# Kernel tuning notes

Hardware: AMD Instinct MI355X
Metric: run time of the kernel (lower is better)

## Reference

```python
import jax, jax.numpy as jnp
import numpy as np

NH, HS = 12, 64            # num heads, head size
H = NH * HS                # hidden size 768
SCALE = 1.0 / np.sqrt(HS)


def binary_quant(x):
    # BinaryQuantizer forward: sign(x)
    return jnp.sign(x)


def zmean_binary_quant(x):
    # ZMeanBinaryQuantizer forward: (sign(x)+1)/2 in {0,1}
    return (jnp.sign(x) + 1.0) * 0.5


def quant_weight(w):
    # 1-bit weight: per-output-row scale * sign(w)
    s = jnp.mean(jnp.abs(w), axis=1, keepdims=True)
    return s * jnp.sign(w)


def setup_inputs() -> dict:
    key = jax.random.key(0)
    ks = jax.random.split(key, 8)
    B, S = 16, 512
    return {
        "hidden_states": jax.random.normal(ks[0], (B, S, H), dtype=jnp.float32),
        "attention_mask": jnp.zeros((B, 1, 1, S), dtype=jnp.float32),
        "Wq": jax.random.normal(ks[1], (H, H), dtype=jnp.float32) * 0.02,
        "bq": jax.random.normal(ks[2], (H,), dtype=jnp.float32) * 0.02,
        "Wk": jax.random.normal(ks[3], (H, H), dtype=jnp.float32) * 0.02,
        "bk": jax.random.normal(ks[4], (H,), dtype=jnp.float32) * 0.02,
        "Wv": jax.random.normal(ks[5], (H, H), dtype=jnp.float32) * 0.02,
        "bv": jax.random.normal(ks[6], (H,), dtype=jnp.float32) * 0.02,
    }


def reference(hidden_states, attention_mask, Wq, bq, Wk, bk, Wv, bv):
    B, S, _ = hidden_states.shape

    def lin(x, W, b):  # F.linear with 1-bit weight
        return x @ quant_weight(W).T + b

    def heads(x):  # [B,S,H] -> [B,NH,S,HS]
        return x.reshape(B, S, NH, HS).transpose(0, 2, 1, 3)

    q = heads(lin(hidden_states, Wq, bq))
    k = heads(lin(hidden_states, Wk, bk))
    v = heads(lin(hidden_states, Wv, bv))

    query_scores = jnp.einsum('bhqd,bhkd->bhqk', q, q) * SCALE
    key_scores = jnp.einsum('bhqd,bhkd->bhqk', k, k) * SCALE

    qb = binary_quant(q)
    kb = binary_quant(k)
    attention_scores = jnp.einsum('bhqd,bhkd->bhqk', qb, kb) * SCALE + attention_mask

    value_scores = jnp.einsum('bhqd,bhkd->bhqk', v, v) * SCALE

    # dropout in eval mode = identity
    attention_probs = zmean_binary_quant(attention_scores)
    vb = binary_quant(v)

    context = jnp.einsum('bhqk,bhkd->bhqd', attention_probs, vb)
    context = context.transpose(0, 2, 1, 3).reshape(B, S, H)
    return (context, attention_scores, value_scores, query_scores, key_scores)
```

## Files before the change

kernel.cpp:

```cpp
#include <hip/hip_runtime.h>
#include <cstdint>

#define B__ 16
#define S__ 512
#define NH__ 12
#define HS__ 64
#define H__ 768
#define BH__ 192
#define M__ 8192
#define K__ 768
#define N3__ 2304
#define PLANE__ 6291456
#define QKV_ELEMS__ 6291456

typedef int    int4v   __attribute__((ext_vector_type(4)));
typedef short  short8  __attribute__((ext_vector_type(8)));
typedef float  float4v __attribute__((ext_vector_type(4)));

__device__ __forceinline__ unsigned short f2bf(float f) {
    unsigned u = __float_as_uint(f);
    u += 0x7fffu + ((u >> 16) & 1u);
    return (unsigned short)(u >> 16);
}

__global__ __launch_bounds__(256)
void prep_w_kernel(const float* __restrict__ Wq, const float* __restrict__ Wk,
                   const float* __restrict__ Wv,
                   double* __restrict__ scales, signed char* __restrict__ sgnW) {
    int wid = threadIdx.x >> 6, lane = threadIdx.x & 63;
    int row = blockIdx.x * 4 + wid;
    if (row >= N3__) return;
    int w = row / 768, i = row - w * 768;
    const float* W = (w == 0) ? Wq : ((w == 1) ? Wk : Wv);
    const float* wr = W + (size_t)i * 768;
    double s = 0.0;
    #pragma unroll
    for (int j = 0; j < 12; j++) {
        float x = wr[lane + j * 64];
        s += fabs((double)x);
        sgnW[(size_t)row * 768 + lane + j * 64] =
            (signed char)((x > 0.f) - (x < 0.f));
    }
    #pragma unroll
    for (int off = 32; off; off >>= 1) s += __shfl_down(s, off);
    if (lane == 0) scales[row] = s * (1.0 / 768.0);
}

__global__ __launch_bounds__(256)
void prep_x_kernel(const float* __restrict__ hs, signed char* __restrict__ planes) {
    int idx = blockIdx.x * 256 + threadIdx.x;
    float x = hs[idx];
    double d = (double)x * 268435456.0;
    d = fmin(fmax(d, -2130706400.0), 2130706400.0);
    int v = __double2int_rn(d);
    int d0 = (int)(signed char)(v & 0xff);
    int r1 = (v - d0) >> 8;
    int d1 = (int)(signed char)(r1 & 0xff);
    int r2 = (r1 - d1) >> 8;
    int d2 = (int)(signed char)(r2 & 0xff);
    int r3 = (r2 - d2) >> 8;
    planes[idx]               = (signed char)d0;
    planes[PLANE__ + idx]     = (signed char)d1;
    planes[2 * PLANE__ + idx] = (signed char)d2;
    planes[3 * PLANE__ + idx] = (signed char)r3;
}

__global__ __launch_bounds__(256)
void proj_kernel(const signed char* __restrict__ planes,
                 const signed char* __restrict__ sgnW,
                 const double* __restrict__ scales,
                 const float* __restrict__ bq, const float* __restrict__ bk,
                 const float* __restrict__ bv,
                 unsigned short* __restrict__ qkv,
                 signed char* __restrict__ qb, signed char* __restrict__ kb,
                 signed char* __restrict__ vbT) {
    int wid = threadIdx.x >> 6, lane = threadIdx.x & 63;
    int lrow = lane & 15, kgrp = lane >> 4;
    int m0 = blockIdx.x * 64 + (wid >> 1) * 32;
    int n0 = blockIdx.y * 64 + (wid & 1) * 32;

    int4v zero = {0, 0, 0, 0};
    int4v acc[2][2][4];
    #pragma unroll
    for (int mt = 0; mt < 2; mt++)
        #pragma unroll
        for (int nt = 0; nt < 2; nt++)
            #pragma unroll
            for (int p = 0; p < 4; p++) acc[mt][nt][p] = zero;

    for (int kc = 0; kc < 12; kc++) {
        int k = kc * 64 + kgrp * 16;
        int4v a[2][4], b[2];
        #pragma unroll
        for (int mt = 0; mt < 2; mt++)
            #pragma unroll
            for (int p = 0; p < 4; p++)
                a[mt][p] = *(const int4v*)(planes + (size_t)p * PLANE__ +
                                           (size_t)(m0 + mt * 16 + lrow) * 768 + k);
        #pragma unroll
        for (int nt = 0; nt < 2; nt++)
            b[nt] = *(const int4v*)(sgnW + (size_t)(n0 + nt * 16 + lrow) * 768 + k);
        #pragma unroll
        for (int mt = 0; mt < 2; mt++)
            #pragma unroll
            for (int nt = 0; nt < 2; nt++)
                #pragma unroll
                for (int p = 0; p < 4; p++)
                    acc[mt][nt][p] = __builtin_amdgcn_mfma_i32_16x16x64_i8(
                        a[mt][p], b[nt], acc[mt][nt][p], 0, 0, 0);
    }

    #pragma unroll
    for (int mt = 0; mt < 2; mt++) {
        #pragma unroll
        for (int nt = 0; nt < 2; nt++) {
            int ng = n0 + nt * 16 + lrow;
            int w = ng / 768;
            int i = ng - w * 768;
            int h = i >> 6, d = i & 63;
            double sc = scales[ng];
            float bias = (w == 0 ? bq : (w == 1 ? bk : bv))[i];
            #pragma unroll
            for (int r = 0; r < 4; r++) {
                long long comb = (long long)acc[mt][nt][0][r]
                               + ((long long)acc[mt][nt][1][r] << 8)
                               + ((long long)acc[mt][nt][2][r] << 16)
                               + ((long long)acc[mt][nt][3][r] << 24);
                int mg = m0 + mt * 16 + kgrp * 4 + r;
                double T = (double)comb * (1.0 / 268435456.0);
                double qv = fma(sc, T, (double)bias);
                int sg = (qv > 0.0) - (qv < 0.0);
                int b_ = mg >> 9, sidx = mg & 511;
                size_t oidx = (((size_t)b_ * NH__ + h) * S__ + sidx) * HS__ + d;
                qkv[(size_t)w * QKV_ELEMS__ + oidx] = f2bf((float)qv);
                if (w == 0)      qb[oidx] = (signed char)sg;
                else if (w == 1) kb[oidx] = (signed char)sg;
                else vbT[((size_t)(b_ * NH__ + h) * HS__ + d) * S__ + sidx] =
                         (signed char)sg;
            }
        }
    }
}

__global__ __launch_bounds__(256)
void score_kernel(const unsigned short* __restrict__ X, float* __restrict__ out) {
    int wid = threadIdx.x >> 6, lane = threadIdx.x & 63;
    int lrow = lane & 15, kgrp = lane >> 4;
    int bh = blockIdx.x;
    int mb = blockIdx.y >> 3, nb = blockIdx.y & 7;
    int m0 = mb * 64 + (wid >> 1) * 32;
    int n0 = nb * 64 + (wid & 1) * 32;
    const unsigned short* Xb = X + (size_t)bh * S__ * HS__;

    float4v acc[2][2];
    #pragma unroll
    for (int mt = 0; mt < 2; mt++)
        #pragma unroll
        for (int nt = 0; nt < 2; nt++) acc[mt][nt] = (float4v){0.f, 0.f, 0.f, 0.f};

    #pragma unroll
    for (int kc = 0; kc < 2; kc++) {
        int k = kc * 32 + kgrp * 8;
        short8 a[2], b[2];
        #pragma unroll
        for (int mt = 0; mt < 2; mt++)
            a[mt] = *(const short8*)(Xb + (size_t)(m0 + mt * 16 + lrow) * HS__ + k);
        #pragma unroll
        for (int nt = 0; nt < 2; nt++)
            b[nt] = *(const short8*)(Xb + (size_t)(n0 + nt * 16 + lrow) * HS__ + k);
        #pragma unroll
        for (int mt = 0; mt < 2; mt++)
            #pragma unroll
            for (int nt = 0; nt < 2; nt++)
                acc[mt][nt] = __builtin_amdgcn_mfma_f32_16x16x32_bf16(
                    a[mt], b[nt], acc[mt][nt], 0, 0, 0);
    }

    float* ob = out + (size_t)bh * S__ * S__;
    #pragma unroll
    for (int mt = 0; mt < 2; mt++)
        #pragma unroll
        for (int nt = 0; nt < 2; nt++)
            #pragma unroll
            for (int r = 0; r < 4; r++)
                ob[(size_t)(m0 + mt * 16 + kgrp * 4 + r) * S__ +
                   n0 + nt * 16 + lrow] = acc[mt][nt][r] * 0.125f;
}

__global__ __launch_bounds__(256)
void attn_kernel(const signed char* __restrict__ qb,
                 const signed char* __restrict__ kb,
                 const signed char* __restrict__ vbT,
                 const float* __restrict__ mask,
                 float* __restrict__ attn_out, float* __restrict__ ctx_out) {
    __shared__ signed char probs2[4][16][528];
    int wid = threadIdx.x >> 6, lane = threadIdx.x & 63;
    int lrow = lane & 15, kgrp = lane >> 4;
    int bh = blockIdx.x;
    int b_ = bh / NH__, h = bh - b_ * NH__;
    int m0 = blockIdx.y * 64 + wid * 16;

    const signed char* qbb = qb + (size_t)bh * S__ * HS__;
    const signed char* kbb = kb + (size_t)bh * S__ * HS__;
    const float* mrow = mask + (size_t)b_ * S__;
    float* ao = attn_out + (size_t)bh * S__ * S__;

    int4v zero = {0, 0, 0, 0};
    int4v afrag = *(const int4v*)(qbb + (size_t)(m0 + lrow) * HS__ + kgrp * 16);

    for (int nt = 0; nt < 32; nt++) {
        int4v bfrag = *(const int4v*)(kbb + (size_t)(nt * 16 + lrow) * HS__ + kgrp * 16);
        int4v dacc = __builtin_amdgcn_mfma_i32_16x16x64_i8(afrag, bfrag, zero, 0, 0, 0);
        #pragma unroll
        for (int r = 0; r < 4; r++) {
            int rowl = kgrp * 4 + r;
            int col = nt * 16 + lrow;
            float sc = (float)dacc[r] * 0.125f + mrow[col];
            ao[(size_t)(m0 + rowl) * S__ + col] = sc;
            probs2[wid][rowl][col] =
                (signed char)(sc > 0.f ? 2 : (sc < 0.f ? 0 : 1));
        }
    }

    const signed char* vt = vbT + (size_t)bh * HS__ * S__;
    int4v acc2[4];
    #pragma unroll
    for (int dt = 0; dt < 4; dt++) acc2[dt] = zero;

    for (int kc = 0; kc < 8; kc++) {
        int k = kc * 64 + kgrp * 16;
        int4v a2 = *(const int4v*)(&probs2[wid][lrow][k]);
        #pragma unroll
        for (int dt = 0; dt < 4; dt++) {
            int4v b2 = *(const int4v*)(vt + (size_t)(dt * 16 + lrow) * S__ + k);
            acc2[dt] = __builtin_amdgcn_mfma_i32_16x16x64_i8(a2, b2, acc2[dt], 0, 0, 0);
        }
    }

    #pragma unroll
    for (int dt = 0; dt < 4; dt++)
        #pragma unroll
        for (int r = 0; r < 4; r++) {
            int srow = m0 + kgrp * 4 + r;
            int d = dt * 16 + lrow;
            ctx_out[((size_t)b_ * S__ + srow) * H__ + h * HS__ + d] =
                (float)acc2[dt][r] * 0.5f;
        }
}

extern "C" void kernel_launch(void* const* d_in, const int* in_sizes, int n_in,
                              void* d_out, int out_size, void* d_ws, size_t ws_size,
                              hipStream_t stream) {
    const float* hs   = (const float*)d_in[0];
    const float* mask = (const float*)d_in[1];
    const float* Wq   = (const float*)d_in[2];
    const float* bq   = (const float*)d_in[3];
    const float* Wk   = (const float*)d_in[4];
    const float* bk   = (const float*)d_in[5];
    const float* Wv   = (const float*)d_in[6];
    const float* bv   = (const float*)d_in[7];

    char* ws = (char*)d_ws;
    double*         scales = (double*)(ws);
    signed char*    sgnW   = (signed char*)(ws + 18432);
    signed char*    planes = (signed char*)(ws + 1787904);
    unsigned short* qkv    = (unsigned short*)(ws + 26953728);
    signed char*    qb     = (signed char*)(ws + 64702464);
    signed char*    kb     = (signed char*)(ws + 70993920);
    signed char*    vbT    = (signed char*)(ws + 77285376);

    float* out  = (float*)d_out;
    float* ctx  = out;
    float* attn = out + 6291456;
    float* vsc  = out + 56623104;
    float* qsc  = out + 106954752;
    float* ksc  = out + 157286400;

    hipLaunchKernelGGL(prep_w_kernel, dim3(576), dim3(256), 0, stream,
                       Wq, Wk, Wv, scales, sgnW);
    hipLaunchKernelGGL(prep_x_kernel, dim3(PLANE__ / 256), dim3(256), 0, stream,
                       hs, planes);
    hipLaunchKernelGGL(proj_kernel, dim3(128, 36), dim3(256), 0, stream,
                       planes, sgnW, scales, bq, bk, bv, qkv, qb, kb, vbT);
    hipLaunchKernelGGL(score_kernel, dim3(192, 64), dim3(256), 0, stream,
                       qkv, qsc);
    hipLaunchKernelGGL(score_kernel, dim3(192, 64), dim3(256), 0, stream,
                       qkv + (size_t)QKV_ELEMS__, ksc);
    hipLaunchKernelGGL(score_kernel, dim3(192, 64), dim3(256), 0, stream,
                       qkv + 2 * (size_t)QKV_ELEMS__, vsc);
    hipLaunchKernelGGL(attn_kernel, dim3(192, 8), dim3(256), 0, stream,
                       qb, kb, vbT, mask, attn, ctx);
}
```

Before: 1.201 ms.

## Swizzle workgroups for XCD locality, merge score launches, vectorize prep_x

```diff
diff --git a/kernel.cpp b/kernel.cpp
--- a/kernel.cpp
+++ b/kernel.cpp
@@ -48,21 +48,29 @@
 
 __global__ __launch_bounds__(256)
 void prep_x_kernel(const float* __restrict__ hs, signed char* __restrict__ planes) {
-    int idx = blockIdx.x * 256 + threadIdx.x;
-    float x = hs[idx];
-    double d = (double)x * 268435456.0;
-    d = fmin(fmax(d, -2130706400.0), 2130706400.0);
-    int v = __double2int_rn(d);
-    int d0 = (int)(signed char)(v & 0xff);
-    int r1 = (v - d0) >> 8;
-    int d1 = (int)(signed char)(r1 & 0xff);
-    int r2 = (r1 - d1) >> 8;
-    int d2 = (int)(signed char)(r2 & 0xff);
-    int r3 = (r2 - d2) >> 8;
-    planes[idx]               = (signed char)d0;
-    planes[PLANE__ + idx]     = (signed char)d1;
-    planes[2 * PLANE__ + idx] = (signed char)d2;
-    planes[3 * PLANE__ + idx] = (signed char)r3;
+    int idx4 = (blockIdx.x * 256 + threadIdx.x) * 4;
+    float4v x4 = *(const float4v*)(hs + idx4);
+    unsigned p0 = 0, p1 = 0, p2 = 0, p3 = 0;
+    #pragma unroll
+    for (int j = 0; j < 4; j++) {
+        double d = (double)x4[j] * 268435456.0;
+        d = fmin(fmax(d, -2130706400.0), 2130706400.0);
+        int v = __double2int_rn(d);
+        int e0 = (int)(signed char)(v & 0xff);
+        int r1 = (v - e0) >> 8;
+        int e1 = (int)(signed char)(r1 & 0xff);
+        int r2 = (r1 - e1) >> 8;
+        int e2 = (int)(signed char)(r2 & 0xff);
+        int r3 = (r2 - e2) >> 8;
+        p0 |= ((unsigned)(unsigned char)e0) << (8 * j);
+        p1 |= ((unsigned)(unsigned char)e1) << (8 * j);
+        p2 |= ((unsigned)(unsigned char)e2) << (8 * j);
+        p3 |= ((unsigned)(unsigned char)(signed char)r3) << (8 * j);
+    }
+    *(unsigned*)(planes + idx4)               = p0;
+    *(unsigned*)(planes + PLANE__ + idx4)     = p1;
+    *(unsigned*)(planes + 2 * PLANE__ + idx4) = p2;
+    *(unsigned*)(planes + 3 * PLANE__ + idx4) = p3;
 }
 
 __global__ __launch_bounds__(256)
@@ -76,8 +84,11 @@
                  signed char* __restrict__ vbT) {
     int wid = threadIdx.x >> 6, lane = threadIdx.x & 63;
     int lrow = lane & 15, kgrp = lane >> 4;
-    int m0 = blockIdx.x * 64 + (wid >> 1) * 32;
-    int n0 = blockIdx.y * 64 + (wid & 1) * 32;
+    int wg = blockIdx.x;
+    int swz = (wg & 7) * 576 + (wg >> 3);
+    int ms = swz / 36, ns = swz - ms * 36;
+    int m0 = ms * 64 + (wid >> 1) * 32;
+    int n0 = ns * 64 + (wid & 1) * 32;
 
     int4v zero = {0, 0, 0, 0};
     int4v acc[2][2][4];
@@ -143,14 +154,22 @@
 }
 
 __global__ __launch_bounds__(256)
-void score_kernel(const unsigned short* __restrict__ X, float* __restrict__ out) {
+void score3_kernel(const unsigned short* __restrict__ qkv,
+                   float* __restrict__ qsc, float* __restrict__ ksc,
+                   float* __restrict__ vsc) {
     int wid = threadIdx.x >> 6, lane = threadIdx.x & 63;
     int lrow = lane & 15, kgrp = lane >> 4;
-    int bh = blockIdx.x;
-    int mb = blockIdx.y >> 3, nb = blockIdx.y & 7;
+    int wg = blockIdx.x;
+    int swz = (wg & 7) * 4608 + (wg >> 3);
+    int z = swz / 12288;
+    int rem = swz - z * 12288;
+    int bh = rem >> 6;
+    int tile = rem & 63;
+    int mb = tile >> 3, nb = tile & 7;
     int m0 = mb * 64 + (wid >> 1) * 32;
     int n0 = nb * 64 + (wid & 1) * 32;
-    const unsigned short* Xb = X + (size_t)bh * S__ * HS__;
+    const unsigned short* Xb =
+        qkv + (size_t)z * QKV_ELEMS__ + (size_t)bh * S__ * HS__;
 
     float4v acc[2][2];
     #pragma unroll
@@ -176,7 +195,7 @@
                     a[mt], b[nt], acc[mt][nt], 0, 0, 0);
     }
 
-    float* ob = out + (size_t)bh * S__ * S__;
+    float* ob = (z == 0 ? qsc : (z == 1 ? ksc : vsc)) + (size_t)bh * S__ * S__;
     #pragma unroll
     for (int mt = 0; mt < 2; mt++)
         #pragma unroll
@@ -196,9 +215,12 @@
     __shared__ signed char probs2[4][16][528];
     int wid = threadIdx.x >> 6, lane = threadIdx.x & 63;
     int lrow = lane & 15, kgrp = lane >> 4;
-    int bh = blockIdx.x;
+    int wg = blockIdx.x;
+    int swz = (wg & 7) * 192 + (wg >> 3);
+    int bh = swz >> 3;
+    int mb = swz & 7;
     int b_ = bh / NH__, h = bh - b_ * NH__;
-    int m0 = blockIdx.y * 64 + wid * 16;
+    int m0 = mb * 64 + wid * 16;
 
     const signed char* qbb = qb + (size_t)bh * S__ * HS__;
     const signed char* kbb = kb + (size_t)bh * S__ * HS__;
@@ -278,16 +300,12 @@
 
     hipLaunchKernelGGL(prep_w_kernel, dim3(576), dim3(256), 0, stream,
                        Wq, Wk, Wv, scales, sgnW);
-    hipLaunchKernelGGL(prep_x_kernel, dim3(PLANE__ / 256), dim3(256), 0, stream,
+    hipLaunchKernelGGL(prep_x_kernel, dim3(PLANE__ / 1024), dim3(256), 0, stream,
                        hs, planes);
-    hipLaunchKernelGGL(proj_kernel, dim3(128, 36), dim3(256), 0, stream,
+    hipLaunchKernelGGL(proj_kernel, dim3(4608), dim3(256), 0, stream,
                        planes, sgnW, scales, bq, bk, bv, qkv, qb, kb, vbT);
-    hipLaunchKernelGGL(score_kernel, dim3(192, 64), dim3(256), 0, stream,
-                       qkv, qsc);
-    hipLaunchKernelGGL(score_kernel, dim3(192, 64), dim3(256), 0, stream,
-                       qkv + (size_t)QKV_ELEMS__, ksc);
-    hipLaunchKernelGGL(score_kernel, dim3(192, 64), dim3(256), 0, stream,
-                       qkv + 2 * (size_t)QKV_ELEMS__, vsc);
-    hipLaunchKernelGGL(attn_kernel, dim3(192, 8), dim3(256), 0, stream,
+    hipLaunchKernelGGL(score3_kernel, dim3(36864), dim3(256), 0, stream,
+                       qkv, qsc, ksc, vsc);
+    hipLaunchKernelGGL(attn_kernel, dim3(1536), dim3(256), 0, stream,
                        qb, kb, vbT, mask, attn, ctx);
 }
```

After: 1.230 ms. 1.02x slower.
